# Kernel tuning notes

Measured on AMD Instinct MI355X. Metric: run time of the kernel, lower is better.

The kernel has to match this reference:

```python
import jax, jax.numpy as jnp
import numpy as np

N = 50000   # num_nodes
H = 128     # n_hidden
C = 16      # num_classes
R = 8       # num_rels
B = 4       # num_bases
E = 800000  # num_edges


def setup_inputs() -> dict:
    key = jax.random.key(0)
    ks = jax.random.split(key, 20)
    s = 0.05
    return {
        "src": jax.random.randint(ks[0], (E,), 0, N),
        "dst": jax.random.randint(ks[1], (E,), 0, N),
        "h": jnp.arange(N),                      # node IDs (first layer in_feat == num_nodes)
        "r": jax.random.randint(ks[2], (E,), 0, R),
        "norm": jax.random.uniform(ks[3], (E, 1), dtype=jnp.float32),
        # layer 0: basis weights over [num_nodes -> H]
        "bases0": jax.random.normal(ks[4], (B, N, H), dtype=jnp.float32) * s,
        "wcomp0": jax.random.normal(ks[5], (R, B), dtype=jnp.float32) * s,
        "loop0": jax.random.normal(ks[6], (N, H), dtype=jnp.float32) * s,
        "bias0": jnp.zeros((H,), dtype=jnp.float32),
        # layer 1: H -> H
        "bases1": jax.random.normal(ks[7], (B, H, H), dtype=jnp.float32) * s,
        "wcomp1": jax.random.normal(ks[8], (R, B), dtype=jnp.float32) * s,
        "loop1": jax.random.normal(ks[9], (H, H), dtype=jnp.float32) * s,
        "bias1": jnp.zeros((H,), dtype=jnp.float32),
        # layer 2: H -> C
        "bases2": jax.random.normal(ks[10], (B, H, C), dtype=jnp.float32) * s,
        "wcomp2": jax.random.normal(ks[11], (R, B), dtype=jnp.float32) * s,
        "loop2": jax.random.normal(ks[12], (H, C), dtype=jnp.float32) * s,
        "bias2": jnp.zeros((C,), dtype=jnp.float32),
    }


def _agg(msg, dst):
    return jax.ops.segment_sum(msg, dst, num_segments=N)


def _layer_id(ids, src, dst, r, norm, bases, wcomp, loop, bias):
    # first layer: input features are node IDs -> embedding lookup into composed weight
    w = jnp.einsum('rb,bnf->rnf', wcomp, bases)      # [R, N, H]
    msg = w[r, ids[src]] * norm                      # [E, H] gather per edge
    out = _agg(msg, dst) + loop[ids] + bias          # aggregate + self-loop + bias
    return jax.nn.relu(out)


def _layer_dense(x, src, dst, r, norm, bases, wcomp, loop, bias, act):
    w = jnp.einsum('rb,bdf->rdf', wcomp, bases)      # [R, d_in, d_out]
    trans = jnp.einsum('nd,rdf->rnf', x, w)          # [R, N, d_out] (all rel transforms)
    msg = trans[r, src] * norm                       # [E, d_out] relation-indexed gather
    out = _agg(msg, dst) + x @ loop + bias
    return jax.nn.relu(out) if act else out


def reference(src, dst, h, r, norm,
              bases0, wcomp0, loop0, bias0,
              bases1, wcomp1, loop1, bias1,
              bases2, wcomp2, loop2, bias2):
    x = _layer_id(h, src, dst, r, norm, bases0, wcomp0, loop0, bias0)
    x = _layer_dense(x, src, dst, r, norm, bases1, wcomp1, loop1, bias1, act=True)
    x = _layer_dense(x, src, dst, r, norm, bases2, wcomp2, loop2, bias2, act=False)
    return x
```

## Files before the change

kernel.cpp:

```cpp
#include <hip/hip_runtime.h>

#define NN 50000
#define NP 50048
#define HH 128
#define CC 16
#define RRL 8
#define BB 4
#define EE 800000
#define NT (RRL * NN)
#define SCAN_CHUNK 2048
#define NBLK_SCAN ((NT + SCAN_CHUNK - 1) / SCAN_CHUNK)
#define KBIG 1152
#define W0B_BLOCKS ((NN * 8 + 255) / 256)
#define COMPOSE_THREADS (HH * KBIG + RRL * CC * HH + CC * HH)
#define COMPOSE_BLOCKS ((COMPOSE_THREADS + 255) / 256)
#define NC 98
#define CAP 10240
#define SPLIT 2
#define CHUNK_E 1024
#define PA_BLOCKS ((EE + CHUNK_E - 1) / CHUNK_E)
#define FRONT_BLOCKS (PA_BLOCKS + W0B_BLOCKS + COMPOSE_BLOCKS)

typedef short bf16x8_t __attribute__((ext_vector_type(8)));
typedef float f32x4_t __attribute__((ext_vector_type(4)));
typedef float f32x2_t __attribute__((ext_vector_type(2)));

__device__ __forceinline__ unsigned short f2bf(float f) {
  unsigned int x = __float_as_uint(f);
  unsigned int r = x + 0x7fffu + ((x >> 16) & 1u);
  return (unsigned short)(r >> 16);
}
__device__ __forceinline__ float bflo(unsigned int u) { return __uint_as_float(u << 16); }
__device__ __forceinline__ float bfhi(unsigned int u) {
  return __uint_as_float(u & 0xffff0000u);
}
__device__ __forceinline__ void acc8v(f32x2_t* a, uint4 v, float nrm) {
  f32x2_t nn = {nrm, nrm};
  f32x2_t u0 = {bflo(v.x), bfhi(v.x)};
  f32x2_t u1 = {bflo(v.y), bfhi(v.y)};
  f32x2_t u2 = {bflo(v.z), bfhi(v.z)};
  f32x2_t u3 = {bflo(v.w), bfhi(v.w)};
  a[0] += nn * u0;
  a[1] += nn * u1;
  a[2] += nn * u2;
  a[3] += nn * u3;
}


__global__ __launch_bounds__(256) void scanA_kernel(const int* __restrict__ cnt,
                                                    int* __restrict__ off,
                                                    int* __restrict__ partials) {
  __shared__ int sums[256];
  int tid = threadIdx.x;
  int base = blockIdx.x * SCAN_CHUNK + tid * 8;
  int v[8];
  int s = 0;
#pragma unroll
  for (int j = 0; j < 8; ++j) {
    int idx = base + j;
    v[j] = (idx < NT) ? cnt[idx] : 0;
    s += v[j];
  }
  sums[tid] = s;
  __syncthreads();
  for (int o = 1; o < 256; o <<= 1) {
    int t = (tid >= o) ? sums[tid - o] : 0;
    __syncthreads();
    sums[tid] += t;
    __syncthreads();
  }
  int run = sums[tid] - s;
#pragma unroll
  for (int j = 0; j < 8; ++j) {
    int idx = base + j;
    if (idx < NT) off[idx] = run;
    run += v[j];
  }
  if (tid == 255) partials[blockIdx.x] = sums[255];
}

__global__ __launch_bounds__(256) void scanB_kernel(const int* __restrict__ partials,
                                                    int* __restrict__ pexcl) {
  __shared__ int sums[256];
  int tid = threadIdx.x;
  int p = (tid < NBLK_SCAN) ? partials[tid] : 0;
  sums[tid] = p;
  __syncthreads();
  for (int o = 1; o < 256; o <<= 1) {
    int t = (tid >= o) ? sums[tid - o] : 0;
    __syncthreads();
    sums[tid] += t;
    __syncthreads();
  }
  if (tid < NBLK_SCAN) pexcl[tid] = sums[tid] - p;
}

__global__ __launch_bounds__(256) void addC_kernel(int* __restrict__ off,
                                                   const int* __restrict__ pexcl,
                                                   int* __restrict__ cur) {
  int tid = threadIdx.x;
  int add = pexcl[blockIdx.x];
  int base = blockIdx.x * SCAN_CHUNK + tid * 8;
#pragma unroll
  for (int j = 0; j < 8; ++j) {
    int idx = base + j;
    if (idx < NT) {
      int v = off[idx] + add;
      off[idx] = v;
      cur[idx] = v;
    }
  }
  if (blockIdx.x == 0 && tid == 0) off[NT] = EE;
}


__global__ __launch_bounds__(256) void front_kernel(
    const int* __restrict__ r, const int* __restrict__ dst, const int* __restrict__ src,
    const int* __restrict__ h, const float* __restrict__ norm, int* __restrict__ cnt2,
    int* __restrict__ tmpCur, unsigned* __restrict__ tmpK, uint2* __restrict__ tmpP,
    unsigned* __restrict__ tmpW, const float* __restrict__ bases0,
    const float* __restrict__ wcomp0, unsigned short* __restrict__ w0b,
    const float* __restrict__ wcomp1, const float* __restrict__ bases1,
    const float* __restrict__ loop1, const float* __restrict__ wcomp2,
    const float* __restrict__ bases2, const float* __restrict__ loop2,
    unsigned short* __restrict__ w1big, unsigned short* __restrict__ w2t,
    unsigned short* __restrict__ loop2t) {
  __shared__ int hist[NC];
  __shared__ int run[NC];
  int tid = threadIdx.x;
  if (blockIdx.x < PA_BLOCKS) {
    int base = blockIdx.x * CHUNK_E;
    for (int i = tid; i < NC; i += 256) hist[i] = 0;
    __syncthreads();
#pragma unroll
    for (int j = 0; j < CHUNK_E / 256; ++j) {
      int e = base + tid + j * 256;
      if (e < EE) atomicAdd(&hist[dst[e] >> 9], 1);
    }
    __syncthreads();
    if (tid < NC && hist[tid] > 0)
      run[tid] = tid * CAP + atomicAdd(&tmpCur[tid], hist[tid]);
    __syncthreads();
#pragma unroll
    for (int j = 0; j < CHUNK_E / 256; ++j) {
      int e = base + tid + j * 256;
      if (e < EE) {
        int d = dst[e], z = r[e];
        int key = d * RRL + z;
        atomicAdd(&cnt2[key], 1);
        int c = d >> 9;
        int pos = atomicAdd(&run[c], 1);
        int sv = src[e];
        tmpK[pos] = (unsigned)key;
        uint2 pay;
        pay.x = (unsigned)sv | ((unsigned)z << 24);
        pay.y = __float_as_uint(norm[e]);
        tmpP[pos] = pay;
        tmpW[pos] = (unsigned)h[sv] * 8u + (unsigned)z;
      }
    }
    return;
  }
  int bx = blockIdx.x - PA_BLOCKS;
  if (bx < W0B_BLOCKS) {
    int idx = bx * 256 + tid;
    int m = idx >> 3, c16 = idx & 7;
    if (m >= NN) return;
    float4 a[BB][4];
#pragma unroll
    for (int b = 0; b < BB; ++b) {
      const float4* sp = (const float4*)(bases0 + ((size_t)b * NN + m) * HH + c16 * 16);
      a[b][0] = sp[0];
      a[b][1] = sp[1];
      a[b][2] = sp[2];
      a[b][3] = sp[3];
    }
    uint4* orow = (uint4*)w0b + (size_t)m * 128 + c16 * 2;
#pragma unroll
    for (int z = 0; z < RRL; ++z) {
      float c0 = wcomp0[z * BB + 0], c1 = wcomp0[z * BB + 1];
      float c2 = wcomp0[z * BB + 2], c3 = wcomp0[z * BB + 3];
      float e[16];
#pragma unroll
      for (int q = 0; q < 4; ++q) {
        e[q * 4 + 0] = c0 * a[0][q].x + c1 * a[1][q].x + c2 * a[2][q].x + c3 * a[3][q].x;
        e[q * 4 + 1] = c0 * a[0][q].y + c1 * a[1][q].y + c2 * a[2][q].y + c3 * a[3][q].y;
        e[q * 4 + 2] = c0 * a[0][q].z + c1 * a[1][q].z + c2 * a[2][q].z + c3 * a[3][q].z;
        e[q * 4 + 3] = c0 * a[0][q].w + c1 * a[1][q].w + c2 * a[2][q].w + c3 * a[3][q].w;
      }
      uint4 pk0, pk1;
      pk0.x = ((unsigned)f2bf(e[1]) << 16) | f2bf(e[0]);
      pk0.y = ((unsigned)f2bf(e[3]) << 16) | f2bf(e[2]);
      pk0.z = ((unsigned)f2bf(e[5]) << 16) | f2bf(e[4]);
      pk0.w = ((unsigned)f2bf(e[7]) << 16) | f2bf(e[6]);
      pk1.x = ((unsigned)f2bf(e[9]) << 16) | f2bf(e[8]);
      pk1.y = ((unsigned)f2bf(e[11]) << 16) | f2bf(e[10]);
      pk1.z = ((unsigned)f2bf(e[13]) << 16) | f2bf(e[12]);
      pk1.w = ((unsigned)f2bf(e[15]) << 16) | f2bf(e[14]);
      orow[z * 16] = pk0;
      orow[z * 16 + 1] = pk1;
    }
    return;
  }
  int idx = (bx - W0B_BLOCKS) * 256 + tid;
  if (idx < HH * KBIG) {
    int n = idx / KBIG, k = idx - n * KBIG;
    float a;
    if (k < 1024) {
      int z = k >> 7, kk = k & 127;
      a = 0.f;
#pragma unroll
      for (int b = 0; b < BB; ++b)
        a += wcomp1[z * BB + b] * bases1[((size_t)b * HH + kk) * HH + n];
    } else {
      int kk = k - 1024;
      a = loop1[kk * HH + n];
    }
    w1big[idx] = f2bf(a);
    return;
  }
  int j = idx - HH * KBIG;
  if (j < RRL * CC * HH) {
    int z = j >> 11;
    int rem = j & 2047;
    int n = rem >> 7, k = rem & 127;
    float a = 0.f;
#pragma unroll
    for (int b = 0; b < BB; ++b)
      a += wcomp2[z * BB + b] * bases2[((size_t)b * HH + k) * CC + n];
    w2t[j] = f2bf(a);
    return;
  }
  j -= RRL * CC * HH;
  if (j < CC * HH) {
    int n = j >> 7, k = j & 127;
    loop2t[j] = f2bf(loop2[k * CC + n]);
  }
}


__global__ __launch_bounds__(256) void placeB_kernel(const int* __restrict__ tmpCur,
                                                     const unsigned* __restrict__ tmpK,
                                                     const uint2* __restrict__ tmpP,
                                                     const unsigned* __restrict__ tmpW,
                                                     int* __restrict__ cur2,
                                                     uint2* __restrict__ ep1,
                                                     uint2* __restrict__ epw) {
  int c = blockIdx.x / SPLIT, q = blockIdx.x % SPLIT;
  int cnt = tmpCur[c];
  int qb = (cnt * q) / SPLIT;
  int qe = (cnt * (q + 1)) / SPLIT;
  int base = c * CAP;
  for (int i = qb + threadIdx.x; i < qe; i += 256) {
    unsigned key = tmpK[base + i];
    uint2 pay = tmpP[base + i];
    unsigned w = tmpW[base + i];
    int pos = atomicAdd(&cur2[key], 1);
    ep1[pos] = pay;
    epw[pos] = (uint2){w, pay.y};
  }
}


__global__ __launch_bounds__(256) void l0_seg_kernel(
    const int* __restrict__ h, const int* __restrict__ off2, const uint2* __restrict__ epw,
    const unsigned short* __restrict__ w0b, const float* __restrict__ loop0,
    const float* __restrict__ bias0, unsigned short* __restrict__ x1b) {
  int lane = threadIdx.x & 63;
  int n = blockIdx.x * 4 + (threadIdx.x >> 6);
  if (n >= NP) return;
  const int g = lane >> 4;
  const int t = lane & 15;
  f32x2_t acc[4];
#pragma unroll
  for (int j = 0; j < 4; ++j) acc[j] = (f32x2_t){0.f, 0.f};

  if (n < NN) {
    int beg = off2[n * RRL];
    int end = off2[n * RRL + RRL];
    int i = beg + g;
    uint2 p0 = {0u, 0u}, p1 = {0u, 0u};
    if (i < end) p0 = epw[i];
    if (i + 4 < end) p1 = epw[i + 4];
    while (i < end) {
      uint2 q0 = {0u, 0u}, q1 = {0u, 0u};
      if (i + 8 < end) q0 = epw[i + 8];
      if (i + 12 < end) q1 = epw[i + 12];
      uint4 va = *(const uint4*)(w0b + (size_t)p0.x * HH + t * 8);
      uint4 vb = *(const uint4*)(w0b + (size_t)p1.x * HH + t * 8);
      acc8v(acc, va, __uint_as_float(p0.y));
      acc8v(acc, vb, __uint_as_float(p1.y));
      i += 8;
      p0 = q0;
      p1 = q1;
    }
  }
  float* af = (float*)acc;
#pragma unroll
  for (int j = 0; j < 8; ++j) {
    af[j] += __shfl_xor(af[j], 16, 64);
    af[j] += __shfl_xor(af[j], 32, 64);
  }
  if (g != 0) return;
  uint4 o = {0u, 0u, 0u, 0u};
  if (n < NN) {
    int hn = h[n];
    float4 l0v = ((const float4*)(loop0 + (size_t)hn * HH))[t * 2];
    float4 l1v = ((const float4*)(loop0 + (size_t)hn * HH))[t * 2 + 1];
    float4 b0v = ((const float4*)bias0)[t * 2];
    float4 b1v = ((const float4*)bias0)[t * 2 + 1];
    float e0 = fmaxf(af[0] + l0v.x + b0v.x, 0.f);
    float e1 = fmaxf(af[1] + l0v.y + b0v.y, 0.f);
    float e2 = fmaxf(af[2] + l0v.z + b0v.z, 0.f);
    float e3 = fmaxf(af[3] + l0v.w + b0v.w, 0.f);
    float e4 = fmaxf(af[4] + l1v.x + b1v.x, 0.f);
    float e5 = fmaxf(af[5] + l1v.y + b1v.y, 0.f);
    float e6 = fmaxf(af[6] + l1v.z + b1v.z, 0.f);
    float e7 = fmaxf(af[7] + l1v.w + b1v.w, 0.f);
    o.x = ((unsigned)f2bf(e1) << 16) | f2bf(e0);
    o.y = ((unsigned)f2bf(e3) << 16) | f2bf(e2);
    o.z = ((unsigned)f2bf(e5) << 16) | f2bf(e4);
    o.w = ((unsigned)f2bf(e7) << 16) | f2bf(e6);
  }
  *(uint4*)(x1b + (size_t)n * HH + t * 8) = o;
}


__global__ __launch_bounds__(256) void l1_agg_kernel(const int* __restrict__ off2,
                                                     const uint2* __restrict__ ep1,
                                                     const unsigned short* __restrict__ x1b,
                                                     unsigned short* __restrict__ AGG) {
  int tid = threadIdx.x;
  int gid = blockIdx.x * 16 + (tid >> 4);
  int l = tid & 15;
  int n = gid >> 3, z = gid & 7;
  if (n >= NP) return;
  unsigned short* orow = AGG + (size_t)n * 1024 + z * 128 + l * 8;
  if (n >= NN) {
    *(uint4*)orow = (uint4){0u, 0u, 0u, 0u};
    return;
  }
  int beg = off2[gid];
  int end = off2[gid + 1];
  f32x2_t a[4];
#pragma unroll
  for (int j = 0; j < 4; ++j) a[j] = (f32x2_t){0.f, 0.f};

  int i = beg;
  uint2 p0 = {0u, 0u}, p1 = {0u, 0u};
  if (i < end) p0 = ep1[i];
  if (i + 1 < end) p1 = ep1[i + 1];
  while (i < end) {
    uint2 q0 = {0u, 0u}, q1 = {0u, 0u};
    if (i + 2 < end) q0 = ep1[i + 2];
    if (i + 3 < end) q1 = ep1[i + 3];
    unsigned s0 = p0.x & 0xFFFFFFu, s1 = p1.x & 0xFFFFFFu;
    uint4 v0 = *(const uint4*)(x1b + (size_t)s0 * HH + l * 8);
    uint4 v1 = *(const uint4*)(x1b + (size_t)s1 * HH + l * 8);
    acc8v(a, v0, __uint_as_float(p0.y));
    acc8v(a, v1, __uint_as_float(p1.y));
    i += 2;
    p0 = q0;
    p1 = q1;
  }
  float* af = (float*)a;
  uint4 o;
  o.x = ((unsigned)f2bf(af[1]) << 16) | f2bf(af[0]);
  o.y = ((unsigned)f2bf(af[3]) << 16) | f2bf(af[2]);
  o.z = ((unsigned)f2bf(af[5]) << 16) | f2bf(af[4]);
  o.w = ((unsigned)f2bf(af[7]) << 16) | f2bf(af[6]);
  *(uint4*)orow = o;
}


__global__ __launch_bounds__(256) void gemm_k1152_kernel(
    const unsigned short* __restrict__ AGG, const unsigned short* __restrict__ x1b,
    const unsigned short* __restrict__ w1big, const float* __restrict__ bias1,
    unsigned short* __restrict__ x2b) {
  constexpr int LP = 136;
  __shared__ unsigned short Alds[64 * LP];
  __shared__ unsigned short Blds[128 * LP];
  const int row0 = blockIdx.x * 64;
  const int tid = threadIdx.x;
  const int w = tid >> 6, lane = tid & 63;
  const int quad = lane >> 4, l15 = lane & 15;
  const int rb = (w >> 1) * 32;
  const int cb = (w & 1) * 64;

  f32x4_t acc[2][4];
#pragma unroll
  for (int rt = 0; rt < 2; ++rt)
#pragma unroll
    for (int ct = 0; ct < 4; ++ct) acc[rt][ct] = (f32x4_t){0.f, 0.f, 0.f, 0.f};

  for (int kb = 0; kb < 9; ++kb) {
    if (kb) __syncthreads();
#pragma unroll
    for (int it = 0; it < 4; ++it) {
      int flat = tid + it * 256;
      int row = flat >> 4, c8 = flat & 15;
      const unsigned short* srcp =
          (kb < 8) ? AGG + (size_t)(row0 + row) * 1024 + kb * 128 + c8 * 8
                   : x1b + (size_t)(row0 + row) * 128 + c8 * 8;
      *(uint4*)(&Alds[row * LP + c8 * 8]) = *(const uint4*)srcp;
    }
#pragma unroll
    for (int it = 0; it < 8; ++it) {
      int flat = tid + it * 256;
      int row = flat >> 4, c8 = flat & 15;
      *(uint4*)(&Blds[row * LP + c8 * 8]) =
          *(const uint4*)(w1big + (size_t)row * KBIG + kb * 128 + c8 * 8);
    }
    __syncthreads();
#pragma unroll
    for (int ks = 0; ks < 4; ++ks) {
      int ko = ks * 32 + quad * 8;
      bf16x8_t af[2], bfr[4];
#pragma unroll
      for (int rt = 0; rt < 2; ++rt)
        af[rt] = *(const bf16x8_t*)(&Alds[(rb + rt * 16 + l15) * LP + ko]);
#pragma unroll
      for (int ct = 0; ct < 4; ++ct)
        bfr[ct] = *(const bf16x8_t*)(&Blds[(cb + ct * 16 + l15) * LP + ko]);
#pragma unroll
      for (int rt = 0; rt < 2; ++rt)
#pragma unroll
        for (int ct = 0; ct < 4; ++ct)
          acc[rt][ct] =
              __builtin_amdgcn_mfma_f32_16x16x32_bf16(af[rt], bfr[ct], acc[rt][ct], 0, 0, 0);
    }
  }
#pragma unroll
  for (int rt = 0; rt < 2; ++rt)
#pragma unroll
    for (int ct = 0; ct < 4; ++ct) {
      int n = cb + ct * 16 + l15;
      float bv = bias1[n];
#pragma unroll
      for (int i = 0; i < 4; ++i) {
        int m = row0 + rb + rt * 16 + quad * 4 + i;
        float val = (m < NN) ? fmaxf(acc[rt][ct][i] + bv, 0.f) : 0.f;
        x2b[(size_t)m * HH + n] = f2bf(val);
      }
    }
}


__global__ __launch_bounds__(256) void l2_trans_kernel(
    const unsigned short* __restrict__ x2b, const unsigned short* __restrict__ w2t,
    const unsigned short* __restrict__ loop2t, const float* __restrict__ bias2,
    unsigned short* __restrict__ trans2, float* __restrict__ out) {
  constexpr int LP = 136;
  __shared__ unsigned short Alds[128 * LP];
  __shared__ unsigned short Blds[9][16 * LP];
  const int row0 = blockIdx.x * 128;
  const int tid = threadIdx.x;

#pragma unroll
  for (int it = 0; it < 8; ++it) {
    int flat = tid + it * 256;
    int row = flat >> 4, c8 = flat & 15;
    *(uint4*)(&Alds[row * LP + c8 * 8]) =
        *(const uint4*)(x2b + ((size_t)(row0 + row)) * 128 + c8 * 8);
  }
  {
    int row = tid >> 4, c8 = tid & 15;
#pragma unroll
    for (int z = 0; z < 9; ++z) {
      const unsigned short* B = (z < 8) ? w2t + (size_t)z * CC * HH : loop2t;
      *(uint4*)(&Blds[z][row * LP + c8 * 8]) = *(const uint4*)(B + row * 128 + c8 * 8);
    }
  }
  __syncthreads();

  const int w = tid >> 6, lane = tid & 63;
  const int quad = lane >> 4, l15 = lane & 15;
  const int rb = w * 32;

  for (int z = 0; z < 9; ++z) {
    f32x4_t acc[2];
    acc[0] = (f32x4_t){0.f, 0.f, 0.f, 0.f};
    acc[1] = (f32x4_t){0.f, 0.f, 0.f, 0.f};
#pragma unroll
    for (int ks = 0; ks < 4; ++ks) {
      int ko = ks * 32 + quad * 8;
      bf16x8_t af0 = *(const bf16x8_t*)(&Alds[(rb + l15) * LP + ko]);
      bf16x8_t af1 = *(const bf16x8_t*)(&Alds[(rb + 16 + l15) * LP + ko]);
      bf16x8_t bfr = *(const bf16x8_t*)(&Blds[z][l15 * LP + ko]);
      acc[0] = __builtin_amdgcn_mfma_f32_16x16x32_bf16(af0, bfr, acc[0], 0, 0, 0);
      acc[1] = __builtin_amdgcn_mfma_f32_16x16x32_bf16(af1, bfr, acc[1], 0, 0, 0);
    }
    if (z < 8) {
      unsigned short* ob = trans2 + (size_t)z * NP * CC;
#pragma unroll
      for (int rt = 0; rt < 2; ++rt)
#pragma unroll
        for (int i = 0; i < 4; ++i) {
          int m = row0 + rb + rt * 16 + quad * 4 + i;
          ob[(size_t)m * CC + l15] = f2bf(acc[rt][i]);
        }
    } else {
      float bv = bias2[l15];
#pragma unroll
      for (int rt = 0; rt < 2; ++rt)
#pragma unroll
        for (int i = 0; i < 4; ++i) {
          int m = row0 + rb + rt * 16 + quad * 4 + i;
          if (m < NN) out[(size_t)m * CC + l15] = acc[rt][i] + bv;
        }
    }
  }
}


__global__ __launch_bounds__(256) void l2_seg_kernel(const int* __restrict__ off2,
                                                     const uint2* __restrict__ ep1,
                                                     const unsigned short* __restrict__ trans2,
                                                     float* __restrict__ outp) {
  int lane = threadIdx.x & 63;
  int n = blockIdx.x * 4 + (threadIdx.x >> 6);
  if (n >= NN) return;
  const int g = lane >> 3;
  const int t = lane & 7;
  float a0 = 0.f, a1 = 0.f;
  int beg = off2[n * RRL];
  int end = off2[n * RRL + RRL];
  int i = beg + g;
  uint2 p0 = {0u, 0u}, p1 = {0u, 0u};
  if (i < end) p0 = ep1[i];
  if (i + 8 < end) p1 = ep1[i + 8];
  while (i < end) {
    uint2 q0 = {0u, 0u}, q1 = {0u, 0u};
    if (i + 16 < end) q0 = ep1[i + 16];
    if (i + 24 < end) q1 = ep1[i + 24];
    unsigned s0 = p0.x & 0xFFFFFFu, z0 = p0.x >> 24;
    unsigned s1 = p1.x & 0xFFFFFFu, z1 = p1.x >> 24;
    unsigned int u0 =
        *(const unsigned int*)(trans2 + ((size_t)z0 * NP + s0) * CC + t * 2);
    unsigned int u1 =
        *(const unsigned int*)(trans2 + ((size_t)z1 * NP + s1) * CC + t * 2);
    float na = __uint_as_float(p0.y), nb = __uint_as_float(p1.y);
    a0 = fmaf(na, bflo(u0), a0);
    a1 = fmaf(na, bfhi(u0), a1);
    a0 = fmaf(nb, bflo(u1), a0);
    a1 = fmaf(nb, bfhi(u1), a1);
    i += 16;
    p0 = q0;
    p1 = q1;
  }
  a0 += __shfl_xor(a0, 8, 64);
  a0 += __shfl_xor(a0, 16, 64);
  a0 += __shfl_xor(a0, 32, 64);
  a1 += __shfl_xor(a1, 8, 64);
  a1 += __shfl_xor(a1, 16, 64);
  a1 += __shfl_xor(a1, 32, 64);
  if (g != 0) return;
  float2* o = (float2*)(outp + (size_t)n * CC) + t;
  float2 cv = *o;
  cv.x += a0;
  cv.y += a1;
  *o = cv;
}


extern "C" void kernel_launch(void* const* d_in, const int* in_sizes, int n_in,
                              void* d_out, int out_size, void* d_ws, size_t ws_size,
                              hipStream_t stream) {
  const int* src = (const int*)d_in[0];
  const int* dst = (const int*)d_in[1];
  const int* h = (const int*)d_in[2];
  const int* r = (const int*)d_in[3];
  const float* norm = (const float*)d_in[4];
  const float* bases0 = (const float*)d_in[5];
  const float* wcomp0 = (const float*)d_in[6];
  const float* loop0 = (const float*)d_in[7];
  const float* bias0 = (const float*)d_in[8];
  const float* bases1 = (const float*)d_in[9];
  const float* wcomp1 = (const float*)d_in[10];
  const float* loop1 = (const float*)d_in[11];
  const float* bias1 = (const float*)d_in[12];
  const float* bases2 = (const float*)d_in[13];
  const float* wcomp2 = (const float*)d_in[14];
  const float* loop2 = (const float*)d_in[15];
  const float* bias2 = (const float*)d_in[16];
  float* out = (float*)d_out;

  char* p = (char*)d_ws;
  auto alloc = [&](size_t bytes) {
    char* q = p;
    p += (bytes + 255) & ~(size_t)255;
    return q;
  };
  unsigned short* x1b = (unsigned short*)alloc((size_t)NP * HH * 2);
  unsigned short* x2b = (unsigned short*)alloc((size_t)NP * HH * 2);
  unsigned short* trans2 = (unsigned short*)alloc((size_t)RRL * NP * CC * 2);
  unsigned short* w1big = (unsigned short*)alloc((size_t)HH * KBIG * 2);
  unsigned short* w2t = (unsigned short*)alloc((size_t)RRL * CC * HH * 2);
  unsigned short* loop2t = (unsigned short*)alloc((size_t)CC * HH * 2);
  uint2* ep1 = (uint2*)alloc((size_t)EE * 8);
  uint2* epw = (uint2*)alloc((size_t)EE * 8);
  unsigned* tmpK = (unsigned*)alloc((size_t)NC * CAP * 4);
  uint2* tmpP = (uint2*)alloc((size_t)NC * CAP * 8);
  unsigned* tmpW = (unsigned*)alloc((size_t)NC * CAP * 4);
  int* off2 = (int*)alloc((size_t)(NT + 1) * 4);
  int* cur2 = (int*)alloc((size_t)NT * 4);
  int* cnt2 = (int*)alloc((size_t)(NT + 256) * 4);
  int* tmpCur = cnt2 + NT;
  int* partials = (int*)alloc(1024);
  int* pexcl = (int*)alloc(1024);
  unsigned short* BIG = (unsigned short*)alloc((size_t)RRL * NP * HH * 2);

  hipMemsetAsync(cnt2, 0, (size_t)(NT + 256) * 4, stream);
  front_kernel<<<FRONT_BLOCKS, 256, 0, stream>>>(
      r, dst, src, h, norm, cnt2, tmpCur, tmpK, tmpP, tmpW, bases0, wcomp0, BIG, wcomp1,
      bases1, loop1, wcomp2, bases2, loop2, w1big, w2t, loop2t);

  scanA_kernel<<<NBLK_SCAN, 256, 0, stream>>>(cnt2, off2, partials);
  scanB_kernel<<<1, 256, 0, stream>>>(partials, pexcl);
  addC_kernel<<<NBLK_SCAN, 256, 0, stream>>>(off2, pexcl, cur2);
  placeB_kernel<<<NC * SPLIT, 256, 0, stream>>>(tmpCur, tmpK, tmpP, tmpW, cur2, ep1, epw);

  l0_seg_kernel<<<NP / 4, 256, 0, stream>>>(h, off2, epw, BIG, loop0, bias0, x1b);

  l1_agg_kernel<<<NP * 8 / 16, 256, 0, stream>>>(off2, ep1, x1b, BIG);
  gemm_k1152_kernel<<<NP / 64, 256, 0, stream>>>(BIG, x1b, w1big, bias1, x2b);

  l2_trans_kernel<<<NP / 128, 256, 0, stream>>>(x2b, w2t, loop2t, bias2, trans2, out);
  l2_seg_kernel<<<(NN + 3) / 4, 256, 0, stream>>>(off2, ep1, trans2, out);
}
```

Before: 472.9 us.

## Fuse layer-1 relation aggregation into the K=1152 GEMM A-tile load

Removes the separate l1_agg kernel that wrote per-relation aggregated bf16 features to a 50048x1024 buffer. The GEMM now computes each 64-row x 128-col A tile on the fly by gathering and summing edge messages straight into LDS, one relation per k-block. This drops a large global write plus re-read and one launch. In exchange the GEMM blocks run irregular gather loops with serialized passes, only 782 blocks, and weight loads that cannot overlap with them, so latency hiding and occupancy may suffer.

```diff
diff --git a/kernel.cpp b/kernel.cpp
--- a/kernel.cpp
+++ b/kernel.cpp
@@ -326,57 +326,10 @@
 }
 
 
-__global__ __launch_bounds__(256) void l1_agg_kernel(const int* __restrict__ off2,
-                                                     const uint2* __restrict__ ep1,
-                                                     const unsigned short* __restrict__ x1b,
-                                                     unsigned short* __restrict__ AGG) {
-  int tid = threadIdx.x;
-  int gid = blockIdx.x * 16 + (tid >> 4);
-  int l = tid & 15;
-  int n = gid >> 3, z = gid & 7;
-  if (n >= NP) return;
-  unsigned short* orow = AGG + (size_t)n * 1024 + z * 128 + l * 8;
-  if (n >= NN) {
-    *(uint4*)orow = (uint4){0u, 0u, 0u, 0u};
-    return;
-  }
-  int beg = off2[gid];
-  int end = off2[gid + 1];
-  f32x2_t a[4];
-#pragma unroll
-  for (int j = 0; j < 4; ++j) a[j] = (f32x2_t){0.f, 0.f};
-
-  int i = beg;
-  uint2 p0 = {0u, 0u}, p1 = {0u, 0u};
-  if (i < end) p0 = ep1[i];
-  if (i + 1 < end) p1 = ep1[i + 1];
-  while (i < end) {
-    uint2 q0 = {0u, 0u}, q1 = {0u, 0u};
-    if (i + 2 < end) q0 = ep1[i + 2];
-    if (i + 3 < end) q1 = ep1[i + 3];
-    unsigned s0 = p0.x & 0xFFFFFFu, s1 = p1.x & 0xFFFFFFu;
-    uint4 v0 = *(const uint4*)(x1b + (size_t)s0 * HH + l * 8);
-    uint4 v1 = *(const uint4*)(x1b + (size_t)s1 * HH + l * 8);
-    acc8v(a, v0, __uint_as_float(p0.y));
-    acc8v(a, v1, __uint_as_float(p1.y));
-    i += 2;
-    p0 = q0;
-    p1 = q1;
-  }
-  float* af = (float*)a;
-  uint4 o;
-  o.x = ((unsigned)f2bf(af[1]) << 16) | f2bf(af[0]);
-  o.y = ((unsigned)f2bf(af[3]) << 16) | f2bf(af[2]);
-  o.z = ((unsigned)f2bf(af[5]) << 16) | f2bf(af[4]);
-  o.w = ((unsigned)f2bf(af[7]) << 16) | f2bf(af[6]);
-  *(uint4*)orow = o;
-}
-
-
 __global__ __launch_bounds__(256) void gemm_k1152_kernel(
-    const unsigned short* __restrict__ AGG, const unsigned short* __restrict__ x1b,
-    const unsigned short* __restrict__ w1big, const float* __restrict__ bias1,
-    unsigned short* __restrict__ x2b) {
+    const int* __restrict__ off2, const uint2* __restrict__ ep1,
+    const unsigned short* __restrict__ x1b, const unsigned short* __restrict__ w1big,
+    const float* __restrict__ bias1, unsigned short* __restrict__ x2b) {
   constexpr int LP = 136;
   __shared__ unsigned short Alds[64 * LP];
   __shared__ unsigned short Blds[128 * LP];
@@ -395,14 +348,53 @@
 
   for (int kb = 0; kb < 9; ++kb) {
     if (kb) __syncthreads();
-#pragma unroll
-    for (int it = 0; it < 4; ++it) {
-      int flat = tid + it * 256;
-      int row = flat >> 4, c8 = flat & 15;
-      const unsigned short* srcp =
-          (kb < 8) ? AGG + (size_t)(row0 + row) * 1024 + kb * 128 + c8 * 8
-                   : x1b + (size_t)(row0 + row) * 128 + c8 * 8;
-      *(uint4*)(&Alds[row * LP + c8 * 8]) = *(const uint4*)srcp;
+    if (kb < 8) {
+      const int l = tid & 15;
+      const int grp = tid >> 4;
+#pragma unroll
+      for (int pass = 0; pass < 4; ++pass) {
+        int row = pass * 16 + grp;
+        int n = row0 + row;
+        f32x2_t a[4];
+#pragma unroll
+        for (int j = 0; j < 4; ++j) a[j] = (f32x2_t){0.f, 0.f};
+        if (n < NN) {
+          int gid = n * RRL + kb;
+          int i = off2[gid];
+          int end = off2[gid + 1];
+          uint2 p0 = {0u, 0u}, p1 = {0u, 0u};
+          if (i < end) p0 = ep1[i];
+          if (i + 1 < end) p1 = ep1[i + 1];
+          while (i < end) {
+            uint2 q0 = {0u, 0u}, q1 = {0u, 0u};
+            if (i + 2 < end) q0 = ep1[i + 2];
+            if (i + 3 < end) q1 = ep1[i + 3];
+            unsigned s0 = p0.x & 0xFFFFFFu, s1 = p1.x & 0xFFFFFFu;
+            uint4 v0 = *(const uint4*)(x1b + (size_t)s0 * HH + l * 8);
+            uint4 v1 = *(const uint4*)(x1b + (size_t)s1 * HH + l * 8);
+            acc8v(a, v0, __uint_as_float(p0.y));
+            acc8v(a, v1, __uint_as_float(p1.y));
+            i += 2;
+            p0 = q0;
+            p1 = q1;
+          }
+        }
+        float* af = (float*)a;
+        uint4 o;
+        o.x = ((unsigned)f2bf(af[1]) << 16) | f2bf(af[0]);
+        o.y = ((unsigned)f2bf(af[3]) << 16) | f2bf(af[2]);
+        o.z = ((unsigned)f2bf(af[5]) << 16) | f2bf(af[4]);
+        o.w = ((unsigned)f2bf(af[7]) << 16) | f2bf(af[6]);
+        *(uint4*)(&Alds[row * LP + l * 8]) = o;
+      }
+    } else {
+#pragma unroll
+      for (int it = 0; it < 4; ++it) {
+        int flat = tid + it * 256;
+        int row = flat >> 4, c8 = flat & 15;
+        *(uint4*)(&Alds[row * LP + c8 * 8]) =
+            *(const uint4*)(x1b + (size_t)(row0 + row) * 128 + c8 * 8);
+      }
     }
 #pragma unroll
     for (int it = 0; it < 8; ++it) {
@@ -622,8 +614,7 @@
 
   l0_seg_kernel<<<NP / 4, 256, 0, stream>>>(h, off2, epw, BIG, loop0, bias0, x1b);
 
-  l1_agg_kernel<<<NP * 8 / 16, 256, 0, stream>>>(off2, ep1, x1b, BIG);
-  gemm_k1152_kernel<<<NP / 64, 256, 0, stream>>>(BIG, x1b, w1big, bias1, x2b);
+  gemm_k1152_kernel<<<NP / 64, 256, 0, stream>>>(off2, ep1, x1b, w1big, bias1, x2b);
 
   l2_trans_kernel<<<NP / 128, 256, 0, stream>>>(x2b, w2t, loop2t, bias2, trans2, out);
   l2_seg_kernel<<<(NN + 3) / 4, 256, 0, stream>>>(off2, ep1, trans2, out);
```

New measurement: 531.6 us. 12.4% more time.
